# Performance work log

Measured on AMD Instinct MI355X. Metric: run time of the kernel, lower is better.

Reference implementation:

```python
import jax, jax.numpy as jnp
import numpy as np

N_NODES, N_EDGES, B, K = 10000, 100000, 8192, 10
MEM = EMB = TE = EF = 172
HID = 80
MSG = 2 * MEM + TE + EF  # 688


def setup_inputs() -> dict:
    key = jax.random.key(0)
    ks = jax.random.split(key, 24)
    f = jax.random.normal
    inp = {
        'timestamps': jax.random.uniform(ks[0], (B,)) * 100.0,
        'edge_features': f(ks[1], (N_EDGES, EF)),
        'temporal_node_features': f(ks[2], (N_NODES, MEM)),
        'node_mem': 0.1 * f(ks[3], (N_NODES, MEM)),
        'last_updated': jax.random.uniform(ks[4], (N_NODES,)) * 50.0,
        'nbr_edge_times': jax.random.uniform(ks[5], (B, K)) * 100.0,
        # TimeEncode params (fixed init from source)
        'time_w': jnp.asarray(1.0 / 10 ** np.linspace(0, 9, TE), jnp.float32),
        'time_b': jnp.zeros((TE,), jnp.float32),
        # RNNCell params
        'rnn_Wih': 0.05 * f(ks[6], (MEM, MSG)),
        'rnn_Whh': 0.05 * f(ks[7], (MEM, MEM)),
        'rnn_bih': jnp.zeros((MEM,)),
        'rnn_bhh': jnp.zeros((MEM,)),
        # layer linears (n_layers=1)
        'lin1_w': 0.05 * f(ks[8], (EMB, EMB + TE + EF)),
        'lin1_b': jnp.zeros((EMB,)),
        'lin2_w': 0.05 * f(ks[9], (EMB, MEM + TE + EMB)),
        'lin2_b': jnp.zeros((EMB,)),
        # MLP head
        'mlp_w1': 0.05 * f(ks[10], (HID, EMB)),
        'mlp_b1': jnp.zeros((HID,)),
        'mlp_w2': 0.05 * f(ks[11], (10, HID)),
        'mlp_b2': jnp.zeros((10,)),
        'mlp_w3': 0.05 * f(ks[12], (1, 10)),
        'mlp_b3': jnp.zeros((1,)),
        'sources': jax.random.randint(ks[13], (B,), 0, N_NODES),
        'destinations': jax.random.randint(ks[14], (B,), 0, N_NODES),
        'edge_idxs': jax.random.randint(ks[15], (B,), 0, N_EDGES),
        'neighbors': jax.random.randint(ks[16], (B, K), 0, N_NODES),
        'nbr_edge_idxs': jax.random.randint(ks[17], (B, K), 0, N_EDGES),
    }
    return inp


def _time_enc(dt, w, b):
    # cos(Linear(1->D)(t)) from TimeEncode
    return jnp.cos(dt[..., None] * w + b)


def reference(timestamps, edge_features, temporal_node_features, node_mem,
              last_updated, nbr_edge_times, time_w, time_b,
              rnn_Wih, rnn_Whh, rnn_bih, rnn_bhh,
              lin1_w, lin1_b, lin2_w, lin2_b,
              mlp_w1, mlp_b1, mlp_w2, mlp_b2, mlp_w3, mlp_b3,
              sources, destinations, edge_idxs, neighbors, nbr_edge_idxs):
    # ---- get_message: gather memories + edge features + time-delta encoding
    ef = edge_features[edge_idxs]                         # [B, EF]
    src_mem = node_mem[sources]                           # [B, MEM]
    dst_mem = node_mem[destinations]                      # [B, MEM]
    dt = timestamps - last_updated[sources]               # [B]
    msg = jnp.concatenate([src_mem, dst_mem, ef, _time_enc(dt, time_w, time_b)], axis=1)  # [B, MSG]

    # ---- message aggregation: keep LAST message per unique source node
    n = node_mem.shape[0]
    b = sources.shape[0]
    last_idx = jnp.full((n,), -1, jnp.int32).at[sources].max(jnp.arange(b, dtype=jnp.int32))
    upd = last_idx >= 0                                   # [N] nodes receiving a message
    gi = jnp.clip(last_idx, 0)
    node_msg = msg[gi]                                    # [N, MSG]

    # ---- RNNCell memory update (masked to updated nodes)
    h_new = jnp.tanh(node_msg @ rnn_Wih.T + rnn_bih + node_mem @ rnn_Whh.T + rnn_bhh)
    mem = jnp.where(upd[:, None], h_new, node_mem)        # [N, MEM]

    # ---- compute_embedding, n_layers = 1 (layer-0 feats = mem + temporal feats)
    src_feat = mem[sources] + temporal_node_features[sources]      # [B, MEM]
    nbr_feat = mem[neighbors] + temporal_node_features[neighbors]  # [B, K, MEM]
    edge_t_enc = _time_enc(timestamps[:, None] - nbr_edge_times, time_w, time_b)  # [B, K, TE]
    nbr_ef = edge_features[nbr_edge_idxs]                           # [B, K, EF]
    nf = jnp.concatenate([nbr_feat, edge_t_enc, nbr_ef], axis=2)    # [B, K, MEM+TE+EF]
    h1 = jnp.einsum('bkf,ef->bke', nf, lin1_w) + lin1_b             # linear_1
    nbr_sum = jax.nn.relu(jnp.sum(h1, axis=1))                      # sum-aggregate, [B, EMB]
    src_t_enc = _time_enc(jnp.zeros_like(timestamps), time_w, time_b)  # cos(b), [B, TE]
    emb = jnp.concatenate([nbr_sum, src_feat, src_t_enc], axis=1) @ lin2_w.T + lin2_b  # [B, EMB]

    # ---- MLP head (dropout disabled / eval mode) + sigmoid
    h = jax.nn.relu(emb @ mlp_w1.T + mlp_b1)
    h = jax.nn.relu(h @ mlp_w2.T + mlp_b2)
    return jax.nn.sigmoid((h @ mlp_w3.T + mlp_b3)[:, 0])  # [B]
```

## Files before the change

kernel.cpp:

```cpp
#include <hip/hip_runtime.h>
#include <math.h>

#define N_NODES 10000
#define BB 8192
#define KK 10
#define D 172
#define HIDD 80

typedef _Float16 f16;
typedef f16 f16x8 __attribute__((ext_vector_type(8)));
typedef f16 f16x4 __attribute__((ext_vector_type(4)));
typedef float f32x4 __attribute__((ext_vector_type(4)));


__global__ void scatter_last(const int* __restrict__ sources, int* __restrict__ last_idx) {
    int b = blockIdx.x * blockDim.x + threadIdx.x;
    if (b < BB) atomicMax(&last_idx[sources[b]], b);
}

__global__ void compact_nodes(const int* __restrict__ last_idx, int* __restrict__ nid,
                              int* __restrict__ li_arr, int* __restrict__ cnt) {
    int n = blockIdx.x * blockDim.x + threadIdx.x;
    if (n < N_NODES) {
        int li = last_idx[n];
        if (li >= 0) { int p = atomicAdd(cnt, 1); nid[p] = n; li_arr[p] = li; }
    }
}

#define CR0 135168
#define CR1 (CR0 + 104448)
#define CR2 (CR1 + 67584)
#define CR3 (CR2 + 15360)
#define CR4 (CR3 + 192)
#define CR5 (CR4 + 220000)
#define CR6 (CR5 + 10001)

__global__ __launch_bounds__(256) void conv_weights(
    const float* __restrict__ Wih, const float* __restrict__ Whh,
    const float* __restrict__ lin1_w, const float* __restrict__ lin2_w,
    const float* __restrict__ w1,
    const float* __restrict__ bih, const float* __restrict__ bhh,
    const float* __restrict__ lin2_b, const float* __restrict__ tb,
    const float* __restrict__ node_mem, const float* __restrict__ tnf,
    f16* __restrict__ Wc, f16* __restrict__ W1, f16* __restrict__ W2,
    f16* __restrict__ Wm1, float* __restrict__ bcomb, float* __restrict__ embc,
    f16* __restrict__ FEAT, int* __restrict__ last_idx, int* __restrict__ cnt)
{
    const int idx = blockIdx.x * 256 + threadIdx.x;
    if (idx < CR0) {
        int n = idx / 704, k = idx % 704, seg = k / 176, kk = k % 176;
        float v = 0.f;
        if (n < D && kk < D) {
            v = Wih[n * 688 + seg * D + kk];
            if (seg == 0) v += Whh[n * D + kk];
        }
        Wc[idx] = (f16)v;
    } else if (idx < CR1) {
        int i = idx - CR0;
        int n = i / 544, k = i % 544, seg = k / 176, kk = k % 176;
        float v = 0.f;
        if (n < D && seg < 3 && kk < D) v = lin1_w[n * 516 + seg * D + kk];
        W1[i] = (f16)v;
    } else if (idx < CR2) {
        int i = idx - CR1;
        int n = i / 352, k = i % 352, seg = k / 176, kk = k % 176;
        float v = 0.f;
        if (n < D && kk < D) v = lin2_w[n * 516 + seg * D + kk];
        W2[i] = (f16)v;
    } else if (idx < CR3) {
        int i = idx - CR2;
        int n = i / 192, k = i % 192;
        Wm1[i] = (f16)((k < D) ? w1[n * D + k] : 0.f);
    } else if (idx < CR4) {
        int i = idx - CR3;
        if (i < D) {
            bcomb[i] = bih[i] + bhh[i];
            float acc = lin2_b[i];
            for (int j = 0; j < D; ++j) acc += lin2_w[i * 516 + 344 + j] * __cosf(tb[j]);
            embc[i] = acc;
        }
    } else if (idx < CR5) {
        int i = idx - CR4;
        int n = i / 22, k0 = (i % 22) * 8;
        f16x8 o;
        #pragma unroll
        for (int j = 0; j < 8; ++j) {
            int kk = k0 + j;
            float v = (kk < D) ? node_mem[(size_t)n * D + kk] + tnf[(size_t)n * D + kk] : 0.f;
            o[j] = (f16)v;
        }
        *(f16x8*)(FEAT + (size_t)n * 176 + k0) = o;
    } else if (idx < CR6) {
        int i = idx - CR5;
        if (i < N_NODES) last_idx[i] = -1;
        else *cnt = 0;
    }
}

#define LDA_R 712

__global__ __launch_bounds__(768) void gemm_rnn_fused(
    const f16* __restrict__ Wc, const float* __restrict__ bcomb,
    const int* __restrict__ nid, const int* __restrict__ li_arr, const int* __restrict__ cnt,
    const int* __restrict__ destinations, const int* __restrict__ edge_idxs,
    const float* __restrict__ timestamps, const float* __restrict__ last_updated,
    const float* __restrict__ node_mem, const float* __restrict__ edge_features,
    const float* __restrict__ tw, const float* __restrict__ tb,
    const float* __restrict__ tnf, f16* __restrict__ FEAT)
{
    const int c = *cnt;
    const int R0 = blockIdx.x * 16;
    if (R0 >= c) return;
    __shared__ f16 As[16 * LDA_R];
    __shared__ int s_n[16], s_dst[16], s_ei[16];
    __shared__ float s_dt[16];
    const int t = threadIdx.x;
    if (t < 16) {
        int i = R0 + t; if (i > c - 1) i = c - 1;
        int n = nid[i], li = li_arr[i];
        s_n[t] = n; s_dst[t] = destinations[li]; s_ei[t] = edge_idxs[li];
        s_dt[t] = timestamps[li] - last_updated[n];
    }
    __syncthreads();
    for (int idx = t; idx < 16 * 88; idx += 768) {
        int row = idx / 88, sub = idx - row * 88;
        int seg = sub / 22, cpos = sub - seg * 22, k0 = cpos * 8;
        f16x8 o;
        if (seg < 3) {
            int n = (seg == 0) ? s_n[row] : (seg == 1) ? s_dst[row] : s_ei[row];
            const float* src = ((seg < 2) ? node_mem : edge_features) + (size_t)n * D + k0;
            float4 lo = *(const float4*)src;
            float4 hi = (cpos < 21) ? *(const float4*)(src + 4) : make_float4(0.f, 0.f, 0.f, 0.f);
            o[0] = (f16)lo.x; o[1] = (f16)lo.y; o[2] = (f16)lo.z; o[3] = (f16)lo.w;
            o[4] = (f16)hi.x; o[5] = (f16)hi.y; o[6] = (f16)hi.z; o[7] = (f16)hi.w;
        } else {
            float dt = s_dt[row];
            #pragma unroll
            for (int j = 0; j < 8; ++j) {
                int kk = k0 + j;
                o[j] = (f16)((kk < D) ? __cosf(dt * tw[kk] + tb[kk]) : 0.f);
            }
        }
        *(f16x8*)(As + row * LDA_R + seg * 176 + k0) = o;
    }
    __syncthreads();
    const int w = t >> 6, l = t & 63;
    if (w >= 11) return;
    const int lane16 = l & 15, koff = (l >> 4) * 8;
    const int C0 = w * 16;
    const f16* Al = As + lane16 * LDA_R + koff;
    const f16* Bp = Wc + (size_t)(C0 + lane16) * 704 + koff;
    f32x4 acc = {};
    #pragma unroll 2
    for (int s = 0; s < 22; ++s) {
        f16x8 a = *(const f16x8*)(Al + s * 32);
        f16x8 b = *(const f16x8*)(Bp + s * 32);
        acc = __builtin_amdgcn_mfma_f32_16x16x32_f16(a, b, acc, 0, 0, 0);
    }
    const int col = C0 + lane16;
    const int rloc = (l >> 4) * 4;
    if (col < D) {
        const float bc = bcomb[col];
        #pragma unroll
        for (int reg = 0; reg < 4; ++reg) {
            int rl = rloc + reg;
            int r = R0 + rl;
            if (r >= c) continue;
            int n = s_n[rl];
            FEAT[(size_t)n * 176 + col] = (f16)(tanhf(acc[reg] + bc) + tnf[(size_t)n * D + col]);
        }
    }
}

#define LDA_1 552
#define LDA_2 360
#define LDE  200

__global__ __launch_bounds__(768) void embed_fused(
    const f16* __restrict__ W1, const float* __restrict__ lin1_b,
    const f16* __restrict__ W2, const float* __restrict__ embc,
    const f16* __restrict__ Wm1, const float* __restrict__ b1,
    const float* __restrict__ w2, const float* __restrict__ b2,
    const float* __restrict__ w3, const float* __restrict__ b3,
    const f16* __restrict__ FEAT, const float* __restrict__ edge_features,
    const float* __restrict__ timestamps, const float* __restrict__ nbr_edge_times,
    const int* __restrict__ neighbors, const int* __restrict__ nbr_edge_idxs,
    const int* __restrict__ sources,
    const float* __restrict__ tw, const float* __restrict__ tb,
    float* __restrict__ out)
{
    __shared__ f16 As[16 * LDA_1];
    __shared__ f16 Acat[16 * LDA_2];
    __shared__ float sH[16][84];
    __shared__ float s_w2[10 * HIDD];
    __shared__ float s_b2[10], s_w3[10], s_b3;
    __shared__ int s_nbr[160], s_nei[160], s_src[16];
    __shared__ float s_net[160], s_ts[16];
    const int t = threadIdx.x;
    const int R0 = blockIdx.x * 16;
    for (int i = t; i < 10 * HIDD; i += 768) s_w2[i] = w2[i];
    if (t < 10) { s_b2[t] = b2[t]; s_w3[t] = w3[t]; }
    if (t == 10) s_b3 = b3[0];
    if (t >= 64 && t < 224) {
        int u = t - 64;
        s_nbr[u] = neighbors[R0 * KK + u];
    } else if (t >= 224 && t < 384) {
        int u = t - 224;
        s_nei[u] = nbr_edge_idxs[R0 * KK + u];
        s_net[u] = nbr_edge_times[R0 * KK + u];
    } else if (t >= 384 && t < 400) {
        s_ts[t - 384] = timestamps[R0 + t - 384];
    } else if (t >= 400 && t < 416) {
        s_src[t - 400] = sources[R0 + t - 400];
    }
    __syncthreads();
    for (int idx = t; idx < 16 * 90 + 16 * 22; idx += 768) {
        if (idx < 16 * 90) {
            int row = idx / 90, c = idx - row * 90;
            if (c < 22) {
                int k0 = c * 8;
                f16x8 v[KK];
                #pragma unroll
                for (int k = 0; k < KK; ++k)
                    v[k] = *(const f16x8*)(FEAT + (size_t)s_nbr[row * KK + k] * 176 + k0);
                float a[8] = {};
                #pragma unroll
                for (int k = 0; k < KK; ++k) {
                    #pragma unroll
                    for (int j = 0; j < 8; ++j) a[j] += (float)v[k][j];
                }
                f16x8 o;
                #pragma unroll
                for (int j = 0; j < 8; ++j) o[j] = (f16)a[j];
                *(f16x8*)(As + row * LDA_1 + k0) = o;
            } else if (c < 44) {
                int k0 = (c - 22) * 8;
                float ts = s_ts[row];
                f16x8 o;
                #pragma unroll
                for (int j = 0; j < 8; ++j) {
                    int kk = k0 + j;
                    float a = 0.f;
                    if (kk < D) {
                        float w = tw[kk], bb = tb[kk];
                        #pragma unroll
                        for (int k = 0; k < KK; ++k) a += __cosf((ts - s_net[row * KK + k]) * w + bb);
                    }
                    o[j] = (f16)a;
                }
                *(f16x8*)(As + row * LDA_1 + 176 + k0) = o;
            } else if (c < 88) {
                int cc = c - 44;
                f16x4 o;
                if (cc == 43) {
                    o[0] = o[1] = o[2] = o[3] = (f16)0.f;
                } else {
                    float4 e[KK];
                    #pragma unroll
                    for (int k = 0; k < KK; ++k)
                        e[k] = *(const float4*)(edge_features + (size_t)s_nei[row * KK + k] * D + cc * 4);
                    float a0 = 0.f, a1 = 0.f, a2 = 0.f, a3 = 0.f;
                    #pragma unroll
                    for (int k = 0; k < KK; ++k) { a0 += e[k].x; a1 += e[k].y; a2 += e[k].z; a3 += e[k].w; }
                    o[0] = (f16)a0; o[1] = (f16)a1; o[2] = (f16)a2; o[3] = (f16)a3;
                }
                *(f16x4*)(As + row * LDA_1 + 352 + cc * 4) = o;
            } else {
                f16x8 z = {};
                *(f16x8*)(As + row * LDA_1 + 528 + (c - 88) * 8) = z;
            }
        } else {
            int j = idx - 16 * 90;
            int row = j / 22, cc = j - row * 22;
            *(f16x8*)(Acat + row * LDA_2 + 176 + cc * 8) =
                *(const f16x8*)(FEAT + (size_t)s_src[row] * 176 + cc * 8);
        }
    }
    __syncthreads();
    const int w = t >> 6, l = t & 63;
    const int lane16 = l & 15, koff = (l >> 4) * 8;
    const int rloc = (l >> 4) * 4;
    const int C0 = w * 16;
    if (w < 11) {
        const f16* Al = As + lane16 * LDA_1 + koff;
        const f16* Bp = W1 + (size_t)(C0 + lane16) * 544 + koff;
        f32x4 acc = {};
        #pragma unroll 2
        for (int s = 0; s < 17; ++s) {
            f16x8 a = *(const f16x8*)(Al + s * 32);
            f16x8 b = *(const f16x8*)(Bp + s * 32);
            acc = __builtin_amdgcn_mfma_f32_16x16x32_f16(a, b, acc, 0, 0, 0);
        }
        const int col = C0 + lane16;
        if (col < 176) {
            const float bb = (col < D) ? 10.0f * lin1_b[col] : 0.f;
            #pragma unroll
            for (int reg = 0; reg < 4; ++reg) {
                int r = rloc + reg;
                Acat[r * LDA_2 + col] = (col < D) ? (f16)fmaxf(acc[reg] + bb, 0.f) : (f16)0.f;
            }
        }
    }
    __syncthreads();
    f16* Emb = As;
    if (w < 11) {
        const f16* Al = Acat + lane16 * LDA_2 + koff;
        const f16* Bp = W2 + (size_t)(C0 + lane16) * 352 + koff;
        f32x4 acc = {};
        #pragma unroll 2
        for (int s = 0; s < 11; ++s) {
            f16x8 a = *(const f16x8*)(Al + s * 32);
            f16x8 b = *(const f16x8*)(Bp + s * 32);
            acc = __builtin_amdgcn_mfma_f32_16x16x32_f16(a, b, acc, 0, 0, 0);
        }
        const int col = C0 + lane16;
        const float ec = (col < D) ? embc[col] : 0.f;
        #pragma unroll
        for (int reg = 0; reg < 4; ++reg) {
            int r = rloc + reg;
            Emb[r * LDE + col] = (col < D) ? (f16)(acc[reg] + ec) : (f16)0.f;
        }
    }
    __syncthreads();
    if (w < 5) {
        const int Cm = w * 16;
        const f16* Bp = Wm1 + (size_t)(Cm + lane16) * 192 + koff;
        const f16* Al = Emb + (lane16) * LDE + koff;
        f32x4 acc = {};
        #pragma unroll
        for (int s = 0; s < 6; ++s) {
            f16x8 a = *(const f16x8*)(Al + s * 32);
            f16x8 b = *(const f16x8*)(Bp + s * 32);
            acc = __builtin_amdgcn_mfma_f32_16x16x32_f16(a, b, acc, 0, 0, 0);
        }
        const int col = Cm + lane16;
        #pragma unroll
        for (int reg = 0; reg < 4; ++reg)
            sH[rloc + reg][col] = fmaxf(acc[reg] + b1[col], 0.f);
    }
    __syncthreads();
    if (t < 16) {
        float h2[10];
        #pragma unroll
        for (int j = 0; j < 10; ++j) h2[j] = s_b2[j];
        for (int f = 0; f < HIDD; ++f) {
            float hv = sH[t][f];
            #pragma unroll
            for (int j = 0; j < 10; ++j) h2[j] = fmaf(hv, s_w2[j * HIDD + f], h2[j]);
        }
        float logit = s_b3;
        #pragma unroll
        for (int j = 0; j < 10; ++j) logit += fmaxf(h2[j], 0.f) * s_w3[j];
        out[R0 + t] = 1.f / (1.f + expf(-logit));
    }
}


extern "C" void kernel_launch(void* const* d_in, const int* in_sizes, int n_in,
                              void* d_out, int out_size, void* d_ws, size_t ws_size,
                              hipStream_t stream) {
    const float* timestamps     = (const float*)d_in[0];
    const float* edge_features  = (const float*)d_in[1];
    const float* tnf            = (const float*)d_in[2];
    const float* node_mem       = (const float*)d_in[3];
    const float* last_updated   = (const float*)d_in[4];
    const float* nbr_edge_times = (const float*)d_in[5];
    const float* time_w         = (const float*)d_in[6];
    const float* time_b         = (const float*)d_in[7];
    const float* Wih            = (const float*)d_in[8];
    const float* Whh            = (const float*)d_in[9];
    const float* bih            = (const float*)d_in[10];
    const float* bhh            = (const float*)d_in[11];
    const float* lin1_w         = (const float*)d_in[12];
    const float* lin1_b         = (const float*)d_in[13];
    const float* lin2_w         = (const float*)d_in[14];
    const float* lin2_b         = (const float*)d_in[15];
    const float* w1             = (const float*)d_in[16];
    const float* b1             = (const float*)d_in[17];
    const float* w2             = (const float*)d_in[18];
    const float* b2             = (const float*)d_in[19];
    const float* w3             = (const float*)d_in[20];
    const float* b3             = (const float*)d_in[21];
    const int* sources          = (const int*)d_in[22];
    const int* destinations     = (const int*)d_in[23];
    const int* edge_idxs        = (const int*)d_in[24];
    const int* neighbors        = (const int*)d_in[25];
    const int* nbr_edge_idxs    = (const int*)d_in[26];
    float* out = (float*)d_out;

    char* p = (char*)d_ws;
    auto bump = [&p](size_t bytes) { char* r = p; p += (bytes + 255) & ~(size_t)255; return r; };
    int* last_idx = (int*)bump(N_NODES * 4);
    int* nid      = (int*)bump(N_NODES * 4);
    int* li_arr   = (int*)bump(N_NODES * 4);
    int* cnt      = (int*)bump(256);
    f16* Wc16     = (f16*)bump((size_t)192 * 704 * 2);
    f16* W1_16    = (f16*)bump((size_t)192 * 544 * 2);
    f16* W2_16    = (f16*)bump((size_t)192 * 352 * 2);
    f16* Wm1_16   = (f16*)bump((size_t)80 * 192 * 2);
    float* bcomb  = (float*)bump(D * 4);
    float* embc   = (float*)bump(D * 4);
    f16* FEAT16   = (f16*)bump((size_t)N_NODES * 176 * 2);

    hipLaunchKernelGGL(conv_weights, dim3((CR6 + 255) / 256), dim3(256), 0, stream,
                       Wih, Whh, lin1_w, lin2_w, w1, bih, bhh, lin2_b, time_b,
                       node_mem, tnf, Wc16, W1_16, W2_16, Wm1_16, bcomb, embc,
                       FEAT16, last_idx, cnt);

    hipLaunchKernelGGL(scatter_last, dim3(BB / 256), dim3(256), 0, stream, sources, last_idx);
    hipLaunchKernelGGL(compact_nodes, dim3((N_NODES + 255) / 256), dim3(256), 0, stream,
                       last_idx, nid, li_arr, cnt);

    hipLaunchKernelGGL(gemm_rnn_fused, dim3((N_NODES + 15) / 16), dim3(768), 0, stream,
                       Wc16, bcomb, nid, li_arr, cnt, destinations, edge_idxs,
                       timestamps, last_updated, node_mem, edge_features,
                       time_w, time_b, tnf, FEAT16);

    hipLaunchKernelGGL(embed_fused, dim3(BB / 16), dim3(768), 0, stream,
                       W1_16, lin1_b, W2_16, embc, Wm1_16, b1, w2, b2, w3, b3,
                       FEAT16, edge_features, timestamps, nbr_edge_times,
                       neighbors, nbr_edge_idxs, sources, time_w, time_b, out);
}
```

Before: 90.54 us.

## Merge weight prep, scatter and compaction into one cooperative kernel

Replaces three separate launches (weight conversion/init, scatter of last source index, node compaction) with a single cooperative kernel that uses grid-wide syncs between phases. The goal is to drop two kernel launch gaps. In exchange the prep phase now runs a grid-stride loop over 256 blocks of 768 threads, fewer threads than before, and grid.sync carries its own barrier cost.

```diff
diff --git a/kernel.cpp b/kernel.cpp
--- a/kernel.cpp
+++ b/kernel.cpp
@@ -1,5 +1,8 @@
 #include <hip/hip_runtime.h>
+#include <hip/hip_cooperative_groups.h>
 #include <math.h>
+
+namespace cg = cooperative_groups;
 
 #define N_NODES 10000
 #define BB 8192
@@ -11,21 +14,6 @@
 typedef f16 f16x8 __attribute__((ext_vector_type(8)));
 typedef f16 f16x4 __attribute__((ext_vector_type(4)));
 typedef float f32x4 __attribute__((ext_vector_type(4)));
-
-
-__global__ void scatter_last(const int* __restrict__ sources, int* __restrict__ last_idx) {
-    int b = blockIdx.x * blockDim.x + threadIdx.x;
-    if (b < BB) atomicMax(&last_idx[sources[b]], b);
-}
-
-__global__ void compact_nodes(const int* __restrict__ last_idx, int* __restrict__ nid,
-                              int* __restrict__ li_arr, int* __restrict__ cnt) {
-    int n = blockIdx.x * blockDim.x + threadIdx.x;
-    if (n < N_NODES) {
-        int li = last_idx[n];
-        if (li >= 0) { int p = atomicAdd(cnt, 1); nid[p] = n; li_arr[p] = li; }
-    }
-}
 
 #define CR0 135168
 #define CR1 (CR0 + 104448)
@@ -35,65 +23,78 @@
 #define CR5 (CR4 + 220000)
 #define CR6 (CR5 + 10001)
 
-__global__ __launch_bounds__(256) void conv_weights(
+__global__ __launch_bounds__(768) void prep_coop(
     const float* __restrict__ Wih, const float* __restrict__ Whh,
     const float* __restrict__ lin1_w, const float* __restrict__ lin2_w,
     const float* __restrict__ w1,
     const float* __restrict__ bih, const float* __restrict__ bhh,
     const float* __restrict__ lin2_b, const float* __restrict__ tb,
     const float* __restrict__ node_mem, const float* __restrict__ tnf,
+    const int* __restrict__ sources,
     f16* __restrict__ Wc, f16* __restrict__ W1, f16* __restrict__ W2,
     f16* __restrict__ Wm1, float* __restrict__ bcomb, float* __restrict__ embc,
-    f16* __restrict__ FEAT, int* __restrict__ last_idx, int* __restrict__ cnt)
+    f16* __restrict__ FEAT, int* __restrict__ last_idx,
+    int* __restrict__ nid, int* __restrict__ li_arr, int* __restrict__ cnt)
 {
-    const int idx = blockIdx.x * 256 + threadIdx.x;
-    if (idx < CR0) {
-        int n = idx / 704, k = idx % 704, seg = k / 176, kk = k % 176;
-        float v = 0.f;
-        if (n < D && kk < D) {
-            v = Wih[n * 688 + seg * D + kk];
-            if (seg == 0) v += Whh[n * D + kk];
-        }
-        Wc[idx] = (f16)v;
-    } else if (idx < CR1) {
-        int i = idx - CR0;
-        int n = i / 544, k = i % 544, seg = k / 176, kk = k % 176;
-        float v = 0.f;
-        if (n < D && seg < 3 && kk < D) v = lin1_w[n * 516 + seg * D + kk];
-        W1[i] = (f16)v;
-    } else if (idx < CR2) {
-        int i = idx - CR1;
-        int n = i / 352, k = i % 352, seg = k / 176, kk = k % 176;
-        float v = 0.f;
-        if (n < D && kk < D) v = lin2_w[n * 516 + seg * D + kk];
-        W2[i] = (f16)v;
-    } else if (idx < CR3) {
-        int i = idx - CR2;
-        int n = i / 192, k = i % 192;
-        Wm1[i] = (f16)((k < D) ? w1[n * D + k] : 0.f);
-    } else if (idx < CR4) {
-        int i = idx - CR3;
-        if (i < D) {
-            bcomb[i] = bih[i] + bhh[i];
-            float acc = lin2_b[i];
-            for (int j = 0; j < D; ++j) acc += lin2_w[i * 516 + 344 + j] * __cosf(tb[j]);
-            embc[i] = acc;
-        }
-    } else if (idx < CR5) {
-        int i = idx - CR4;
-        int n = i / 22, k0 = (i % 22) * 8;
-        f16x8 o;
-        #pragma unroll
-        for (int j = 0; j < 8; ++j) {
-            int kk = k0 + j;
-            float v = (kk < D) ? node_mem[(size_t)n * D + kk] + tnf[(size_t)n * D + kk] : 0.f;
-            o[j] = (f16)v;
-        }
-        *(f16x8*)(FEAT + (size_t)n * 176 + k0) = o;
-    } else if (idx < CR6) {
-        int i = idx - CR5;
-        if (i < N_NODES) last_idx[i] = -1;
-        else *cnt = 0;
+    cg::grid_group grid = cg::this_grid();
+    const int t = threadIdx.x;
+    for (int idx = blockIdx.x * 768 + t; idx < CR6; idx += 256 * 768) {
+        if (idx < CR0) {
+            int n = idx / 704, k = idx % 704, seg = k / 176, kk = k % 176;
+            float v = 0.f;
+            if (n < D && kk < D) {
+                v = Wih[n * 688 + seg * D + kk];
+                if (seg == 0) v += Whh[n * D + kk];
+            }
+            Wc[idx] = (f16)v;
+        } else if (idx < CR1) {
+            int i = idx - CR0;
+            int n = i / 544, k = i % 544, seg = k / 176, kk = k % 176;
+            float v = 0.f;
+            if (n < D && seg < 3 && kk < D) v = lin1_w[n * 516 + seg * D + kk];
+            W1[i] = (f16)v;
+        } else if (idx < CR2) {
+            int i = idx - CR1;
+            int n = i / 352, k = i % 352, seg = k / 176, kk = k % 176;
+            float v = 0.f;
+            if (n < D && kk < D) v = lin2_w[n * 516 + seg * D + kk];
+            W2[i] = (f16)v;
+        } else if (idx < CR3) {
+            int i = idx - CR2;
+            int n = i / 192, k = i % 192;
+            Wm1[i] = (f16)((k < D) ? w1[n * D + k] : 0.f);
+        } else if (idx < CR4) {
+            int i = idx - CR3;
+            if (i < D) {
+                bcomb[i] = bih[i] + bhh[i];
+                float acc = lin2_b[i];
+                for (int j = 0; j < D; ++j) acc += lin2_w[i * 516 + 344 + j] * __cosf(tb[j]);
+                embc[i] = acc;
+            }
+        } else if (idx < CR5) {
+            int i = idx - CR4;
+            int n = i / 22, k0 = (i % 22) * 8;
+            f16x8 o;
+            #pragma unroll
+            for (int j = 0; j < 8; ++j) {
+                int kk = k0 + j;
+                float v = (kk < D) ? node_mem[(size_t)n * D + kk] + tnf[(size_t)n * D + kk] : 0.f;
+                o[j] = (f16)v;
+            }
+            *(f16x8*)(FEAT + (size_t)n * 176 + k0) = o;
+        } else {
+            int i = idx - CR5;
+            if (i < N_NODES) last_idx[i] = -1;
+            else *cnt = 0;
+        }
+    }
+    grid.sync();
+    for (int b = blockIdx.x * 768 + t; b < BB; b += 256 * 768)
+        atomicMax(&last_idx[sources[b]], b);
+    grid.sync();
+    for (int n = blockIdx.x * 768 + t; n < N_NODES; n += 256 * 768) {
+        int li = last_idx[n];
+        if (li >= 0) { int p = atomicAdd(cnt, 1); nid[p] = n; li_arr[p] = li; }
     }
 }
 
@@ -402,14 +403,15 @@
     float* embc   = (float*)bump(D * 4);
     f16* FEAT16   = (f16*)bump((size_t)N_NODES * 176 * 2);
 
-    hipLaunchKernelGGL(conv_weights, dim3((CR6 + 255) / 256), dim3(256), 0, stream,
-                       Wih, Whh, lin1_w, lin2_w, w1, bih, bhh, lin2_b, time_b,
-                       node_mem, tnf, Wc16, W1_16, W2_16, Wm1_16, bcomb, embc,
-                       FEAT16, last_idx, cnt);
-
-    hipLaunchKernelGGL(scatter_last, dim3(BB / 256), dim3(256), 0, stream, sources, last_idx);
-    hipLaunchKernelGGL(compact_nodes, dim3((N_NODES + 255) / 256), dim3(256), 0, stream,
-                       last_idx, nid, li_arr, cnt);
+    void* args[] = {
+        (void*)&Wih, (void*)&Whh, (void*)&lin1_w, (void*)&lin2_w, (void*)&w1,
+        (void*)&bih, (void*)&bhh, (void*)&lin2_b, (void*)&time_b,
+        (void*)&node_mem, (void*)&tnf, (void*)&sources,
+        (void*)&Wc16, (void*)&W1_16, (void*)&W2_16, (void*)&Wm1_16,
+        (void*)&bcomb, (void*)&embc, (void*)&FEAT16, (void*)&last_idx,
+        (void*)&nid, (void*)&li_arr, (void*)&cnt
+    };
+    hipLaunchCooperativeKernel((const void*)prep_coop, dim3(256), dim3(768), args, 0, stream);
 
     hipLaunchKernelGGL(gemm_rnn_fused, dim3((N_NODES + 15) / 16), dim3(768), 0, stream,
                        Wc16, bcomb, nid, li_arr, cnt, destinations, edge_idxs,
```

Measured after the change: 156.4 us. 72.7% more time.
